# Kernel tuning notes

Measured on AMD Instinct MI355X. Metric: run time of the kernel, lower is better.

Reference implementation:

```python
import jax, jax.numpy as jnp
import numpy as np

# Multi-scale feature pyramid (H, W) per level: strides 8/16/32/64 on a ~512px image
SHAPES = ((64, 64), (32, 32), (16, 16), (8, 8))
N_HEADS, N_LEVELS, N_POINTS = 8, 4, 4
D_MODEL = 256
HEAD_DIM = D_MODEL // N_HEADS


def setup_inputs() -> dict:
    key = jax.random.key(0)
    ks = jax.random.split(key, 11)
    B, C = 4, D_MODEL
    Lv = sum(h * w for h, w in SHAPES)  # 5440
    Lq = Lv  # encoder self-attention: queries are the flattened features
    scale = 0.02
    return {
        "query": jax.random.normal(ks[0], (B, Lq, C), jnp.float32),
        "reference_points": jax.random.uniform(ks[1], (B, Lq, N_LEVELS, 2), jnp.float32),
        "value": jax.random.normal(ks[2], (B, Lv, C), jnp.float32),
        "W_off": jax.random.normal(ks[3], (C, N_HEADS * N_LEVELS * N_POINTS * 2), jnp.float32) * scale,
        "b_off": jax.random.normal(ks[4], (N_HEADS * N_LEVELS * N_POINTS * 2,), jnp.float32) * 0.5,
        "W_attn": jax.random.normal(ks[5], (C, N_HEADS * N_LEVELS * N_POINTS), jnp.float32) * scale,
        "b_attn": jax.random.normal(ks[6], (N_HEADS * N_LEVELS * N_POINTS,), jnp.float32) * scale,
        "W_val": jax.random.normal(ks[7], (C, C), jnp.float32) * scale,
        "b_val": jax.random.normal(ks[8], (C,), jnp.float32) * scale,
        "W_out": jax.random.normal(ks[9], (C, C), jnp.float32) * scale,
        "b_out": jax.random.normal(ks[10], (C,), jnp.float32) * scale,
    }


def _bilinear_sample(val, grid, H, W):
    """Replicates F.grid_sample(mode='bilinear', padding_mode='zeros', align_corners=False).

    val:  [N, C, H, W]
    grid: [N, Lq, P, 2] in [-1, 1] (x, y order)
    returns: [N, C, Lq, P]
    """
    N, C = val.shape[0], val.shape[1]
    # unnormalize (align_corners=False)
    x = (grid[..., 0] + 1.0) * 0.5 * W - 0.5  # [N, Lq, P]
    y = (grid[..., 1] + 1.0) * 0.5 * H - 0.5
    x0 = jnp.floor(x)
    y0 = jnp.floor(y)
    wx = x - x0  # fractional parts
    wy = y - y0
    flat = val.reshape(N, C, H * W)

    def gather(xi, yi):
        valid = (xi >= 0) & (xi < W) & (yi >= 0) & (yi < H)
        xc = jnp.clip(xi, 0, W - 1).astype(jnp.int32)
        yc = jnp.clip(yi, 0, H - 1).astype(jnp.int32)
        idx = yc * W + xc  # [N, Lq, P]
        g = jax.vmap(lambda v, i: v[:, i])(flat, idx)  # [N, C, Lq, P]
        return g * valid[:, None, :, :].astype(val.dtype)

    out = (gather(x0, y0) * ((1 - wx) * (1 - wy))[:, None]
           + gather(x0 + 1, y0) * (wx * (1 - wy))[:, None]
           + gather(x0, y0 + 1) * ((1 - wx) * wy)[:, None]
           + gather(x0 + 1, y0 + 1) * (wx * wy)[:, None])
    return out


def _ms_deform_attn(query, reference_points, value, W_off, b_off, W_attn, b_attn,
                    W_val, b_val, W_out, b_out):
    B, Lq, C = query.shape
    val = value @ W_val + b_val  # [B, Lv, C]
    val = val.reshape(B, -1, N_HEADS, HEAD_DIM)

    offsets = (query @ W_off + b_off).reshape(B, Lq, N_HEADS, N_LEVELS, N_POINTS, 2)
    weights = jax.nn.softmax(
        (query @ W_attn + b_attn).reshape(B, Lq, N_HEADS, N_LEVELS * N_POINTS), axis=-1
    ).reshape(B, Lq, N_HEADS, N_LEVELS, N_POINTS)

    # offset normalizer: (W, H) per level
    offset_norm = jnp.array([[w, h] for h, w in SHAPES], jnp.float32)
    # ref_dim == 2 branch
    locs = reference_points[:, :, None, :, None, :] + offsets / offset_norm[None, None, None, :, None, :]
    grids = 2.0 * locs - 1.0  # [B, Lq, nh, nl, np, 2]

    acc = jnp.zeros((B * N_HEADS, HEAD_DIM, Lq), query.dtype)
    start = 0
    for lid, (H, W) in enumerate(SHAPES):
        # [B, HW, nh, hd] -> [B*nh, hd, H, W]
        v = val[:, start:start + H * W].transpose(0, 2, 3, 1).reshape(B * N_HEADS, HEAD_DIM, H, W)
        g = grids[:, :, :, lid].transpose(0, 2, 1, 3, 4).reshape(B * N_HEADS, Lq, N_POINTS, 2)
        s = _bilinear_sample(v, g, H, W)  # [B*nh, hd, Lq, np]
        w = weights[:, :, :, lid].transpose(0, 2, 1, 3).reshape(B * N_HEADS, 1, Lq, N_POINTS)
        acc = acc + (s * w).sum(-1)
        start += H * W

    out = acc.reshape(B, D_MODEL, Lq).transpose(0, 2, 1)  # [B, Lq, C]
    return out @ W_out + b_out


def reference(query, reference_points, value, W_off, b_off, W_attn, b_attn,
              W_val, b_val, W_out, b_out):
    return _ms_deform_attn(query, reference_points, value, W_off, b_off,
                           W_attn, b_attn, W_val, b_val, W_out, b_out)
```

## Files before the change

### kernel.cpp

```cpp
#include <hip/hip_runtime.h>


typedef __attribute__((ext_vector_type(8))) _Float16 half8;
typedef __attribute__((ext_vector_type(4))) _Float16 half4;
typedef __attribute__((ext_vector_type(4))) float f32x4;

typedef __attribute__((address_space(3))) unsigned int lds_uint;
typedef const __attribute__((address_space(1))) unsigned int g_uint;

__device__ __forceinline__ void load_lds16(const _Float16* g, _Float16* l) {
    __builtin_amdgcn_global_load_lds((g_uint*)g, (lds_uint*)l, 16, 0, 0);
}

__device__ __forceinline__ half8 splat8(_Float16 v) {
    half8 r = {v, v, v, v, v, v, v, v};
    return r;
}

#define M_TOTAL 21760

__global__ __launch_bounds__(256) void prep_w(
    const float* __restrict__ W_val, const float* __restrict__ W_off,
    const float* __restrict__ W_attn, _Float16* __restrict__ wtf)
{
    const int slot = blockIdx.x * 256 + threadIdx.x;
    const int T = slot >> 11;
    const int rem = slot & 2047;
    const int g = rem >> 6, nl = rem & 63;
    half8 h;
#pragma unroll
    for (int e = 0; e < 8; ++e) {
        const int k = g * 8 + e;
        float v;
        if (T < 4) {
            v = W_val[k * 256 + T * 64 + nl];
        } else {
            const int n2 = (T - 4) * 64 + nl;
            v = (n2 < 256) ? W_off[k * 256 + n2] : W_attn[k * 128 + (n2 - 256)];
        }
        h[e] = (_Float16)v;
    }
    *(half8*)(wtf + ((size_t)slot << 3)) = h;
}

__global__ __launch_bounds__(256) void gemm12_cvt(
    const float* __restrict__ value, const float* __restrict__ query,
    const _Float16* __restrict__ wtf,
    const float* __restrict__ b_val, const float* __restrict__ b_off,
    const float* __restrict__ b_attn,
    _Float16* __restrict__ valh, _Float16* __restrict__ offh)
{
    __shared__ _Float16 Afs[32 * 64 * 8];
    __shared__ _Float16 Bfs[32 * 64 * 8];

    const bool g1 = blockIdx.x < 1360;
    const int id = g1 ? blockIdx.x : blockIdx.x - 1360;
    const int mt = g1 ? (id >> 2) : (id / 6);
    const int nt = g1 ? (id & 3) : (id % 6);
    const int NN = g1 ? 256 : 384;
    const float* A = g1 ? value : query;
    _Float16* C = g1 ? valh : offh;
    const int bm = mt * 64;
    const int bn = nt * 64;
    const int T  = g1 ? nt : 4 + nt;

    const int tid = threadIdx.x;
    const int wave = tid >> 6, lane = tid & 63;
    const int ml = lane & 15, q = lane >> 4;

    const _Float16* wsrc = wtf + ((size_t)T << 14);
#pragma unroll
    for (int i = 0; i < 8; ++i)
        load_lds16(wsrc + (((size_t)i * 256 + tid) << 3),
                   Bfs + (((size_t)i * 256 + wave * 64) << 3));

    {
        const int r = tid >> 2, c4 = tid & 3;
        const float* ap = A + (size_t)(bm + r) * 256 + c4 * 64;
        float4 pa[16];
#pragma unroll
        for (int j = 0; j < 16; ++j) pa[j] = *(const float4*)(ap + j * 4);
#pragma unroll
        for (int u = 0; u < 8; ++u) {
            const float4 a0 = pa[2 * u], a1 = pa[2 * u + 1];
            const half8 h = {(_Float16)a0.x, (_Float16)a0.y, (_Float16)a0.z, (_Float16)a0.w,
                             (_Float16)a1.x, (_Float16)a1.y, (_Float16)a1.z, (_Float16)a1.w};
            *(half8*)(Afs + (((c4 * 8 + u) * 64 + r) << 3)) = h;
        }
    }
    __syncthreads();

    const f32x4 zero4 = {0.f, 0.f, 0.f, 0.f};
    f32x4 acc[4] = {zero4, zero4, zero4, zero4};

#pragma unroll
    for (int kt = 0; kt < 8; ++kt) {
        const int g = kt * 4 + q;
        const half8 af = *(const half8*)(Afs + (((size_t)g * 64 + wave * 16 + ml) << 3));
#pragma unroll
        for (int j = 0; j < 4; ++j) {
            const half8 bf = *(const half8*)(Bfs + (((size_t)g * 64 + j * 16 + ml) << 3));
            acc[j] = __builtin_amdgcn_mfma_f32_16x16x32_f16(af, bf, acc[j], 0, 0, 0);
        }
    }

    const int r0 = q * 4;
#pragma unroll
    for (int j = 0; j < 4; ++j) {
        const int col = bn + j * 16 + ml;
        const float bj = g1 ? b_val[col] : (col < 256 ? b_off[col] : b_attn[col - 256]);
        const size_t rbase = (size_t)(bm + wave * 16 + r0) * NN + col;
#pragma unroll
        for (int r = 0; r < 4; ++r)
            C[rbase + (size_t)r * NN] = (_Float16)(acc[j][r] + bj);
    }
}

__device__ __forceinline__ void gemm_core(
    const _Float16* __restrict__ A, const _Float16* __restrict__ Bt,
    const float* __restrict__ bias, float* __restrict__ Cv,
    int NN, int mt, int nt)
{
    __shared__ _Float16 Ah[128 * 32];
    __shared__ _Float16 Bh[64 * 32];

    const int tid = threadIdx.x;
    const int bm = mt * 128;
    const int bn = nt * 64;
    const int wave = tid >> 6, lane = tid & 63;
    const int wm = (wave & 1) * 64, wn = (wave >> 1) * 32;
    const int ml = lane & 15, kq = (lane >> 4) * 8;
    const int lr = lane >> 2;
    const int lk = (lane & 3) * 8;

    const f32x4 zero4 = {0.f, 0.f, 0.f, 0.f};
    f32x4 acc[4][2];
#pragma unroll
    for (int i = 0; i < 4; ++i)
#pragma unroll
        for (int j = 0; j < 2; ++j) acc[i][j] = zero4;

    for (int kt = 0; kt < 8; ++kt) {
        const int k0 = kt * 32;
        __syncthreads();
#pragma unroll
        for (int t = 0; t < 2; ++t) {
            const int row = wave * 32 + t * 16;
            load_lds16(A + (size_t)(bm + row + lr) * 256 + k0 + lk,
                       Ah + (size_t)row * 32);
        }
        {
            const int row = wave * 16;
            load_lds16(Bt + (size_t)(bn + row + lr) * 256 + k0 + lk,
                       Bh + (size_t)row * 32);
        }
        __syncthreads();

        half8 af[4], bf[2];
#pragma unroll
        for (int i = 0; i < 4; ++i)
            af[i] = *(const half8*)(Ah + (wm + i * 16 + ml) * 32 + kq);
#pragma unroll
        for (int j = 0; j < 2; ++j)
            bf[j] = *(const half8*)(Bh + (wn + j * 16 + ml) * 32 + kq);
#pragma unroll
        for (int i = 0; i < 4; ++i)
#pragma unroll
            for (int j = 0; j < 2; ++j)
                acc[i][j] = __builtin_amdgcn_mfma_f32_16x16x32_f16(af[i], bf[j], acc[i][j], 0, 0, 0);
    }

    const int r0 = (lane >> 4) * 4;
#pragma unroll
    for (int j = 0; j < 2; ++j) {
        const int col = bn + wn + j * 16 + ml;
        const float bj = bias[col];
#pragma unroll
        for (int i = 0; i < 4; ++i) {
            const size_t rbase = (size_t)(bm + wm + i * 16 + r0) * NN + col;
#pragma unroll
            for (int r = 0; r < 4; ++r)
                Cv[rbase + (size_t)r * NN] = acc[i][j][r] + bj;
        }
    }
}

__global__ __launch_bounds__(256) void gemm_single(
    const _Float16* __restrict__ A, const _Float16* __restrict__ Bt,
    const float* __restrict__ bias, float* __restrict__ Cv)
{
    const int id = blockIdx.x;
    gemm_core(A, Bt, bias, Cv, 256, id >> 2, id & 3);
}

__global__ __launch_bounds__(256, 4) void sample_f16(
    const _Float16* __restrict__ valh,
    const float* __restrict__ refp,
    const _Float16* __restrict__ offh,
    const float* __restrict__ W_out,
    _Float16* __restrict__ wto,
    _Float16* __restrict__ acc_out)
{
    if (blockIdx.x < 256)
        wto[blockIdx.x * 256 + threadIdx.x] =
            (_Float16)W_out[threadIdx.x * 256 + blockIdx.x];

    const int wave = threadIdx.x >> 6, lane = threadIdx.x & 63;
    const int q2 = lane >> 5, sl = lane & 31;
    const int bq = blockIdx.x * 8 + wave * 2 + q2;
    const int b = bq / 5440;
    const int h = sl >> 2;
    const int t = sl & 3;
    const int d8 = t * 8;

    const int Wt = 64 >> t;
    const float fW = (float)Wt;

    const half8 ofr = *(const half8*)(offh + (size_t)bq * 384 + h * 32 + t * 8);
    const half4 lgt = *(const half4*)(offh + (size_t)bq * 384 + 256 + h * 16 + t * 4);
    const float2 rxy = *(const float2*)(refp + (size_t)bq * 8 + t * 2);

    float lg[4];
#pragma unroll
    for (int p = 0; p < 4; ++p) lg[p] = (float)lgt[p];

    float mx = fmaxf(fmaxf(lg[0], lg[1]), fmaxf(lg[2], lg[3]));
    mx = fmaxf(mx, __shfl_xor(mx, 1));
    mx = fmaxf(mx, __shfl_xor(mx, 2));
    float s = 0.f;
#pragma unroll
    for (int p = 0; p < 4; ++p) { lg[p] = __expf(lg[p] - mx); s += lg[p]; }
    s += __shfl_xor(s, 1);
    s += __shfl_xor(s, 2);
    const float inv = 1.f / s;

    unsigned pk[16];
#pragma unroll
    for (int p = 0; p < 4; ++p) {
        const float aw = lg[p] * inv;
        const float ox = (float)ofr[p * 2];
        const float oy = (float)ofr[p * 2 + 1];
        const float x = fmaf(rxy.x, fW, ox) - 0.5f;
        const float y = fmaf(rxy.y, fW, oy) - 0.5f;
        const float x0f = floorf(x), y0f = floorf(y);
        const int x0 = (int)x0f, y0 = (int)y0f;
        const float wx = x - x0f, wy = y - y0f;
        const bool okx0 = ((unsigned)x0 < (unsigned)Wt);
        const bool okx1 = ((unsigned)(x0 + 1) < (unsigned)Wt);
        const bool oky0 = ((unsigned)y0 < (unsigned)Wt);
        const bool oky1 = ((unsigned)(y0 + 1) < (unsigned)Wt);
        const int xc0 = min(max(x0, 0), Wt - 1);
        const int xc1 = min(max(x0 + 1, 0), Wt - 1);
        const int yc0 = min(max(y0, 0), Wt - 1);
        const int yc1 = min(max(y0 + 1, 0), Wt - 1);
        const _Float16 w0 = (_Float16)((okx0 & oky0) ? (1.f - wx) * (1.f - wy) * aw : 0.f);
        const _Float16 w1 = (_Float16)((okx1 & oky0) ? wx * (1.f - wy) * aw : 0.f);
        const _Float16 w2 = (_Float16)((okx0 & oky1) ? (1.f - wx) * wy * aw : 0.f);
        const _Float16 w3 = (_Float16)((okx1 & oky1) ? wx * wy * aw : 0.f);
        pk[p * 4 + 0] = ((unsigned)(yc0 * Wt + xc0) << 16) |
                        (unsigned)__builtin_bit_cast(unsigned short, w0);
        pk[p * 4 + 1] = ((unsigned)(yc0 * Wt + xc1) << 16) |
                        (unsigned)__builtin_bit_cast(unsigned short, w1);
        pk[p * 4 + 2] = ((unsigned)(yc1 * Wt + xc0) << 16) |
                        (unsigned)__builtin_bit_cast(unsigned short, w2);
        pk[p * 4 + 3] = ((unsigned)(yc1 * Wt + xc1) << 16) |
                        (unsigned)__builtin_bit_cast(unsigned short, w3);
    }

    const int starts_[4] = {0, 4096, 5120, 5376};
    const int gbase = lane & ~3;

    half8 acc = splat8((_Float16)0.f);
#pragma unroll
    for (int l = 0; l < 4; ++l) {
        const _Float16* vbase = valh + ((size_t)(b * 5440 + starts_[l])) * 256 + h * 32 + d8;
        const int src = gbase + l;

        unsigned q_[16];
#pragma unroll
        for (int c = 0; c < 16; ++c)
            q_[c] = (unsigned)__shfl((int)pk[c], src);

        __builtin_amdgcn_sched_barrier(0);
        half8 c_[16];
#pragma unroll
        for (int c = 0; c < 16; ++c)
            c_[c] = *(const half8*)(vbase + ((size_t)(q_[c] >> 16) << 8));
        __builtin_amdgcn_sched_barrier(0);
#pragma unroll
        for (int c = 0; c < 16; ++c)
            acc += c_[c] * splat8(__builtin_bit_cast(_Float16, (unsigned short)(q_[c] & 0xffffu)));
    }

    *(half8*)(acc_out + (size_t)bq * 256 + h * 32 + d8) = acc;
}

extern "C" void kernel_launch(void* const* d_in, const int* in_sizes, int n_in,
                              void* d_out, int out_size, void* d_ws, size_t ws_size,
                              hipStream_t stream) {
    const float* query  = (const float*)d_in[0];
    const float* refp   = (const float*)d_in[1];
    const float* value  = (const float*)d_in[2];
    const float* W_off  = (const float*)d_in[3];
    const float* b_off  = (const float*)d_in[4];
    const float* W_attn = (const float*)d_in[5];
    const float* b_attn = (const float*)d_in[6];
    const float* W_val  = (const float*)d_in[7];
    const float* b_val  = (const float*)d_in[8];
    const float* W_out  = (const float*)d_in[9];
    const float* b_out  = (const float*)d_in[10];
    float* out = (float*)d_out;

    const size_t M = M_TOTAL;

    _Float16* valh  = (_Float16*)d_ws;
    _Float16* offh  = valh + M * 256;
    _Float16* acc16 = offh + M * 384;
    _Float16* wto   = acc16 + M * 256;
    _Float16* wtf   = wto + 256 * 256;

    dim3 blk(256);
    prep_w<<<dim3(80), blk, 0, stream>>>(W_val, W_off, W_attn, wtf);
    gemm12_cvt<<<dim3(3400), blk, 0, stream>>>(
        value, query, wtf, b_val, b_off, b_attn, valh, offh);
    sample_f16<<<dim3(M / 8), blk, 0, stream>>>(valh, refp, offh, W_out, wto, acc16);
    gemm_single<<<dim3(680), blk, 0, stream>>>(acc16, wto, b_out, out);
}
```

Baseline: 196.8 us.

## Load GEMM B fragments from global, swizzle A in LDS, remap block order

The first GEMM no longer stages the prepacked fp16 weight tile in LDS. Each wave reads its B fragments straight from global memory (expected to hit L2) through a double-buffered register prefetch. Each wave also converts its own 16 rows of A into an XOR-swizzled LDS layout, which lets the block-wide barrier be dropped, and block IDs are remapped modulo 8, likely to spread work across XCDs. This cuts LDS traffic, LDS footprint and barrier cost, in exchange for more global/L2 reads of the weights and higher register pressure.

```diff
diff --git a/kernel.cpp b/kernel.cpp
--- a/kernel.cpp
+++ b/kernel.cpp
@@ -50,11 +50,12 @@
     const float* __restrict__ b_attn,
     _Float16* __restrict__ valh, _Float16* __restrict__ offh)
 {
-    __shared__ _Float16 Afs[32 * 64 * 8];
-    __shared__ _Float16 Bfs[32 * 64 * 8];
-
-    const bool g1 = blockIdx.x < 1360;
-    const int id = g1 ? blockIdx.x : blockIdx.x - 1360;
+    __shared__ _Float16 Asw[64 * 256];
+
+    const int bid = ((int)blockIdx.x % 8) * 425 + ((int)blockIdx.x / 8);
+
+    const bool g1 = bid < 1360;
+    const int id = g1 ? bid : bid - 1360;
     const int mt = g1 ? (id >> 2) : (id / 6);
     const int nt = g1 ? (id & 3) : (id % 6);
     const int NN = g1 ? 256 : 384;
@@ -68,51 +69,67 @@
     const int wave = tid >> 6, lane = tid & 63;
     const int ml = lane & 15, q = lane >> 4;
 
-    const _Float16* wsrc = wtf + ((size_t)T << 14);
-#pragma unroll
-    for (int i = 0; i < 8; ++i)
-        load_lds16(wsrc + (((size_t)i * 256 + tid) << 3),
-                   Bfs + (((size_t)i * 256 + wave * 64) << 3));
-
-    {
-        const int r = tid >> 2, c4 = tid & 3;
-        const float* ap = A + (size_t)(bm + r) * 256 + c4 * 64;
-        float4 pa[16];
-#pragma unroll
-        for (int j = 0; j < 16; ++j) pa[j] = *(const float4*)(ap + j * 4);
-#pragma unroll
-        for (int u = 0; u < 8; ++u) {
-            const float4 a0 = pa[2 * u], a1 = pa[2 * u + 1];
-            const half8 h = {(_Float16)a0.x, (_Float16)a0.y, (_Float16)a0.z, (_Float16)a0.w,
-                             (_Float16)a1.x, (_Float16)a1.y, (_Float16)a1.z, (_Float16)a1.w};
-            *(half8*)(Afs + (((c4 * 8 + u) * 64 + r) << 3)) = h;
-        }
-    }
-    __syncthreads();
+    const int rbase = wave * 16;
+    float4 pa[16];
+#pragma unroll
+    for (int rr = 0; rr < 16; ++rr)
+        pa[rr] = *(const float4*)(A + (size_t)(bm + rbase + rr) * 256 + lane * 4);
+#pragma unroll
+    for (int rr = 0; rr < 16; ++rr) {
+        const int row = rbase + rr;
+        const float4 v = pa[rr];
+        const half4 h = {(_Float16)v.x, (_Float16)v.y, (_Float16)v.z, (_Float16)v.w};
+        const int wbyte = row * 512 + ((lane * 8) ^ ((row & 7) << 4));
+        *(half4*)(Asw + (wbyte >> 1)) = h;
+    }
+
+    const _Float16* bptr = wtf + ((size_t)T << 14) + q * 512 + ml * 8;
+    const int arow = rbase + ml;
+    const int abase = arow * 512;
+    const int swl = (ml & 7) << 4;
 
     const f32x4 zero4 = {0.f, 0.f, 0.f, 0.f};
     f32x4 acc[4] = {zero4, zero4, zero4, zero4};
-
-#pragma unroll
-    for (int kt = 0; kt < 8; ++kt) {
-        const int g = kt * 4 + q;
-        const half8 af = *(const half8*)(Afs + (((size_t)g * 64 + wave * 16 + ml) << 3));
-#pragma unroll
-        for (int j = 0; j < 4; ++j) {
-            const half8 bf = *(const half8*)(Bfs + (((size_t)g * 64 + j * 16 + ml) << 3));
-            acc[j] = __builtin_amdgcn_mfma_f32_16x16x32_f16(af, bf, acc[j], 0, 0, 0);
-        }
-    }
+    half8 bf0[4], bf1[4], af0, af1;
+
+#define BFLOAD(dst, kt)                                                        \
+    {                                                                          \
+        _Pragma("unroll") for (int j = 0; j < 4; ++j)                          \
+            dst[j] = *(const half8*)(bptr + (kt) * 2048 + j * 128);            \
+    }
+#define AFLOAD(kt) \
+    (*(const half8*)(Asw + ((abase + (((kt) * 64 + q * 16) ^ swl)) >> 1)))
+#define MSTEP(bf, af)                                                          \
+    {                                                                          \
+        _Pragma("unroll") for (int j = 0; j < 4; ++j)                          \
+            acc[j] = __builtin_amdgcn_mfma_f32_16x16x32_f16(af, bf[j],         \
+                                                            acc[j], 0, 0, 0); \
+    }
+
+    BFLOAD(bf0, 0); BFLOAD(bf1, 1);
+    af0 = AFLOAD(0);
+    af1 = AFLOAD(1); MSTEP(bf0, af0); BFLOAD(bf0, 2);
+    af0 = AFLOAD(2); MSTEP(bf1, af1); BFLOAD(bf1, 3);
+    af1 = AFLOAD(3); MSTEP(bf0, af0); BFLOAD(bf0, 4);
+    af0 = AFLOAD(4); MSTEP(bf1, af1); BFLOAD(bf1, 5);
+    af1 = AFLOAD(5); MSTEP(bf0, af0); BFLOAD(bf0, 6);
+    af0 = AFLOAD(6); MSTEP(bf1, af1); BFLOAD(bf1, 7);
+    af1 = AFLOAD(7); MSTEP(bf0, af0);
+    MSTEP(bf1, af1);
+
+#undef BFLOAD
+#undef AFLOAD
+#undef MSTEP
 
     const int r0 = q * 4;
 #pragma unroll
     for (int j = 0; j < 4; ++j) {
         const int col = bn + j * 16 + ml;
         const float bj = g1 ? b_val[col] : (col < 256 ? b_off[col] : b_attn[col - 256]);
-        const size_t rbase = (size_t)(bm + wave * 16 + r0) * NN + col;
+        const size_t rbaseC = (size_t)(bm + rbase + r0) * NN + col;
 #pragma unroll
         for (int r = 0; r < 4; ++r)
-            C[rbase + (size_t)r * NN] = (_Float16)(acc[j][r] + bj);
+            C[rbaseC + (size_t)r * NN] = (_Float16)(acc[j][r] + bj);
     }
 }
 
```

Result: faster. 178.6 us (-9.2%).

## Switch gemm12 LDS tiles to XOR-swizzled row-major layout with coalesced A loads

Applied to the files above, without the earlier changes.

Moves the pre-converted weight buffer and the A tile in LDS from a k-group-major layout to a row-major layout with an XOR swizzle on 16-byte chunks, so MFMA fragment reads avoid bank conflicts. The A tile is now loaded with each wave reading whole rows contiguously (lane*4 floats), giving fully coalesced global loads. It also remaps block IDs so that blocks are interleaved across 8 groups, aiming for better spread of work across XCDs or caches. This adds index arithmetic, and the prep kernel and the consumer kernel must agree on the swizzle.

```diff
diff --git a/kernel.cpp b/kernel.cpp
--- a/kernel.cpp
+++ b/kernel.cpp
@@ -26,21 +26,23 @@
     const int slot = blockIdx.x * 256 + threadIdx.x;
     const int T = slot >> 11;
     const int rem = slot & 2047;
-    const int g = rem >> 6, nl = rem & 63;
+    const int n = rem >> 5;
+    const int k0 = (rem & 31) * 8;
     half8 h;
 #pragma unroll
     for (int e = 0; e < 8; ++e) {
-        const int k = g * 8 + e;
+        const int k = k0 + e;
         float v;
         if (T < 4) {
-            v = W_val[k * 256 + T * 64 + nl];
+            v = W_val[k * 256 + T * 64 + n];
         } else {
-            const int n2 = (T - 4) * 64 + nl;
+            const int n2 = (T - 4) * 64 + n;
             v = (n2 < 256) ? W_off[k * 256 + n2] : W_attn[k * 128 + (n2 - 256)];
         }
         h[e] = (_Float16)v;
     }
-    *(half8*)(wtf + ((size_t)slot << 3)) = h;
+    const int dbyte = T * 32768 + n * 512 + ((k0 * 2) ^ ((n & 7) << 4));
+    *(half8*)(wtf + (dbyte >> 1)) = h;
 }
 
 __global__ __launch_bounds__(256) void gemm12_cvt(
@@ -50,11 +52,13 @@
     const float* __restrict__ b_attn,
     _Float16* __restrict__ valh, _Float16* __restrict__ offh)
 {
-    __shared__ _Float16 Afs[32 * 64 * 8];
-    __shared__ _Float16 Bfs[32 * 64 * 8];
-
-    const bool g1 = blockIdx.x < 1360;
-    const int id = g1 ? blockIdx.x : blockIdx.x - 1360;
+    __shared__ _Float16 Asw[64 * 256];
+    __shared__ _Float16 Bsw[64 * 256];
+
+    const int bid = ((int)blockIdx.x % 8) * 425 + ((int)blockIdx.x / 8);
+
+    const bool g1 = bid < 1360;
+    const int id = g1 ? bid : bid - 1360;
     const int mt = g1 ? (id >> 2) : (id / 6);
     const int nt = g1 ? (id & 3) : (id % 6);
     const int NN = g1 ? 256 : 384;
@@ -72,34 +76,37 @@
 #pragma unroll
     for (int i = 0; i < 8; ++i)
         load_lds16(wsrc + (((size_t)i * 256 + tid) << 3),
-                   Bfs + (((size_t)i * 256 + wave * 64) << 3));
-
-    {
-        const int r = tid >> 2, c4 = tid & 3;
-        const float* ap = A + (size_t)(bm + r) * 256 + c4 * 64;
-        float4 pa[16];
-#pragma unroll
-        for (int j = 0; j < 16; ++j) pa[j] = *(const float4*)(ap + j * 4);
-#pragma unroll
-        for (int u = 0; u < 8; ++u) {
-            const float4 a0 = pa[2 * u], a1 = pa[2 * u + 1];
-            const half8 h = {(_Float16)a0.x, (_Float16)a0.y, (_Float16)a0.z, (_Float16)a0.w,
-                             (_Float16)a1.x, (_Float16)a1.y, (_Float16)a1.z, (_Float16)a1.w};
-            *(half8*)(Afs + (((c4 * 8 + u) * 64 + r) << 3)) = h;
-        }
-    }
+                   Bsw + (((size_t)i * 256 + wave * 64) << 3));
+
+    const int rbase = wave * 16;
+    float4 pa[16];
+#pragma unroll
+    for (int rr = 0; rr < 16; ++rr)
+        pa[rr] = *(const float4*)(A + (size_t)(bm + rbase + rr) * 256 + lane * 4);
+#pragma unroll
+    for (int rr = 0; rr < 16; ++rr) {
+        const int row = rbase + rr;
+        const float4 v = pa[rr];
+        const half4 h = {(_Float16)v.x, (_Float16)v.y, (_Float16)v.z, (_Float16)v.w};
+        const int wbyte = row * 512 + ((lane * 8) ^ ((row & 7) << 4));
+        *(half4*)(Asw + (wbyte >> 1)) = h;
+    }
+
     __syncthreads();
+
+    const int swl = (ml & 7) << 4;
+    const int abase = (rbase + ml) * 512;
 
     const f32x4 zero4 = {0.f, 0.f, 0.f, 0.f};
     f32x4 acc[4] = {zero4, zero4, zero4, zero4};
 
 #pragma unroll
     for (int kt = 0; kt < 8; ++kt) {
-        const int g = kt * 4 + q;
-        const half8 af = *(const half8*)(Afs + (((size_t)g * 64 + wave * 16 + ml) << 3));
+        const int koff = (kt * 64 + q * 16) ^ swl;
+        const half8 af = *(const half8*)(Asw + ((abase + koff) >> 1));
 #pragma unroll
         for (int j = 0; j < 4; ++j) {
-            const half8 bf = *(const half8*)(Bfs + (((size_t)g * 64 + j * 16 + ml) << 3));
+            const half8 bf = *(const half8*)(Bsw + ((((j * 16 + ml) * 512) + koff) >> 1));
             acc[j] = __builtin_amdgcn_mfma_f32_16x16x32_f16(af, bf, acc[j], 0, 0, 0);
         }
     }
@@ -109,10 +116,10 @@
     for (int j = 0; j < 4; ++j) {
         const int col = bn + j * 16 + ml;
         const float bj = g1 ? b_val[col] : (col < 256 ? b_off[col] : b_attn[col - 256]);
-        const size_t rbase = (size_t)(bm + wave * 16 + r0) * NN + col;
+        const size_t rbaseC = (size_t)(bm + rbase + r0) * NN + col;
 #pragma unroll
         for (int r = 0; r < 4; ++r)
-            C[rbase + (size_t)r * NN] = (_Float16)(acc[j][r] + bj);
+            C[rbaseC + (size_t)r * NN] = (_Float16)(acc[j][r] + bj);
     }
 }
 
```

After: 178.9 us. -9.1%, faster.
